# Performance work log

Hardware: AMD Instinct MI355X
Metric: run time of the kernel (lower is better)

Reference implementation:

```python
import jax, jax.numpy as jnp
import numpy as np

GRID_SIZE = 128
GAMMA = 200.0


def make_coordinate_grid(dim):
    # meshgrid over [-1, 1] x [-1, 1], shape [G, G, 2] with (x, y) ordering
    x = jnp.arange(dim, dtype=jnp.float32)
    y = jnp.arange(dim, dtype=jnp.float32)
    xx = jnp.broadcast_to(x[None, :], (dim, dim))
    yy = jnp.broadcast_to(y[:, None], (dim, dim))
    meshed = jnp.stack([xx, yy], axis=-1) / (dim - 1) * 2.0 - 1.0
    return meshed  # [G, G, 2]


def distance_transform(kps, mask, grid, gamma):
    # kps: [N, 2] points, mask: [N] bool (True -> segment dropped), grid: [G, G, 2]
    pi = kps[:-1]                      # [S, 2] segment start
    pj = kps[1:]                       # [S, 2] segment end
    v = pi - pj                        # [S, 2]
    u = grid[None, :, :, :] - pj[:, None, None, :]          # [S, G, G, 2]
    uv = jnp.einsum('sghd,sd->sgh', u, v)                   # [S, G, G]
    v_norm = jnp.sum(v * v, axis=-1)                        # [S]
    zero_seg = v_norm == 0.0
    v_safe = jnp.where(zero_seg, 1.0, v_norm)
    # clamp projection to [0,1]; degenerate segments (v_norm==0) fall back to uv
    # (which is exactly 0 there), matching torch's NaN masked_scatter fixup.
    rs = jnp.where(zero_seg[:, None, None], uv,
                   jnp.clip(uv / v_safe[:, None, None], 0.0, 1.0))  # [S, G, G]
    diff = u - rs[..., None] * v[:, None, None, :]          # [S, G, G, 2]
    betas = jnp.exp(-gamma * jnp.sum(diff * diff, axis=-1)) # [S, G, G]
    keep = (~mask[:-1]).astype(betas.dtype)                 # [S]
    betas = betas * keep[:, None, None]
    return jnp.max(betas, axis=0)                           # [G, G]


def setup_inputs() -> dict:
    key = jax.random.key(0)
    k1, k2, k3, k4 = jax.random.split(key, 4)
    N = 2048
    pred_xy = jax.random.uniform(k1, (N, 2), dtype=jnp.float32)
    pred_pen = (jax.random.uniform(k2, (N, 1)) < 0.1).astype(jnp.float32)
    gt_xy = jax.random.uniform(k3, (N, 2), dtype=jnp.float32)
    gt_pen = (jax.random.uniform(k4, (N, 1)) < 0.1).astype(jnp.float32)
    pred_coords = jnp.concatenate([pred_xy, pred_pen], axis=-1)  # [N, 3]
    gt_coords = jnp.concatenate([gt_xy, gt_pen], axis=-1)        # [N, 3]
    return {"pred_coords": pred_coords, "gt_coords": gt_coords}


def reference(pred_coords, gt_coords):
    grid = make_coordinate_grid(GRID_SIZE)
    mask_gt = gt_coords[:, -1] != 0.0
    gt_c = (gt_coords[:, :-1] - 0.5) * 2.0
    mask_pred = pred_coords[:, -1] > 0.5
    pred_c = (pred_coords[:, :-1] - 0.5) * 2.0
    gt_dist = distance_transform(gt_c, mask_gt, grid, GAMMA)
    pred_dist = distance_transform(pred_c, mask_pred, grid, GAMMA)
    dist_loss = jnp.mean((pred_dist - gt_dist) ** 2)
    return dist_loss
```

## Files before the change

kernel.cpp:

```cpp
#include <hip/hip_runtime.h>
#include <math.h>

#define GRID_DIM 128
#define NPIX 16384
#define NSEG 2047
#define NCHUNK 8
#define CHUNK 256
#define NTILE 64
#define GAMMA4 800.0f

typedef float v2f __attribute__((ext_vector_type(2)));


__global__ __launch_bounds__(256) void dist_min_kernel(
    const float* __restrict__ pred, const float* __restrict__ gt,
    unsigned int* __restrict__ ws_min)
{
    __shared__ float4 sA[2][CHUNK / 2];
    __shared__ float4 sB[2][CHUNK / 2];
    __shared__ float2 sC[2][CHUNK / 2];

    const int tid = threadIdx.x;
    const int bx = blockIdx.x;
    const int chunk = blockIdx.y;

    #pragma unroll
    for (int slot = tid; slot < 2 * CHUNK; slot += 256) {
        const int t = slot >> 8;
        const int sl = slot & (CHUNK - 1);
        const int s = chunk * CHUNK + sl;
        float pjx, pjy, vx, vy, inv;
        if (s < NSEG) {
            const float* src = t ? gt : pred;
            const float pix_ = src[3 * s + 0];
            const float piy_ = src[3 * s + 1];
            const float pen  = src[3 * s + 2];
            pjx = src[3 * s + 3];
            pjy = src[3 * s + 4];
            const bool masked = t ? (pen != 0.0f) : (pen > 0.5f);
            vx = pix_ - pjx;
            vy = piy_ - pjy;
            const float vn = vx * vx + vy * vy;
            inv = (vn == 0.0f) ? 0.0f : (1.0f / vn);
            if (masked) { pjx = 1e15f; pjy = 1e15f; vx = 0.0f; vy = 0.0f; inv = 0.0f; }
        } else {
            pjx = 1e15f; pjy = 1e15f; vx = 0.0f; vy = 0.0f; inv = 0.0f;
        }
        float* a = (float*)&sA[t][sl >> 1];
        float* b = (float*)&sB[t][sl >> 1];
        float* c = (float*)&sC[t][sl >> 1];
        const int k = sl & 1;
        a[k] = pjx; a[2 + k] = pjy;
        b[k] = vx;  b[2 + k] = vy;
        c[k] = inv;
    }
    __syncthreads();

    const int p = bx * 256 + tid;
    const float gx = (float)(p & (GRID_DIM - 1)) * (1.0f / 127.0f);
    const float gy = (float)(p >> 7) * (1.0f / 127.0f);
    const v2f gx2 = {gx, gx}, gy2 = {gy, gy};

    #pragma unroll
    for (int t = 0; t < 2; ++t) {
        float m = 3.0e38f;
        #pragma unroll 8
        for (int i = 0; i < CHUNK / 2; ++i) {
            const float4 A = sA[t][i];
            const float4 B = sB[t][i];
            const float2 C = sC[t][i];
            const v2f bx2 = {B.x, B.y}, by2 = {B.z, B.w};
            v2f ux = gx2 - (v2f){A.x, A.y};
            v2f uy = gy2 - (v2f){A.z, A.w};
            v2f uv = ux * bx2 + uy * by2;
            v2f rs = uv * (v2f){C.x, C.y};
            rs.x = fminf(fmaxf(rs.x, 0.0f), 1.0f);
            rs.y = fminf(fmaxf(rs.y, 0.0f), 1.0f);
            v2f dx = ux - rs * bx2;
            v2f dy = uy - rs * by2;
            v2f d2 = dx * dx + dy * dy;
            m = fminf(m, fminf(d2.x, d2.y));
        }
        atomicMin(&ws_min[t * NPIX + p], __float_as_uint(m));
    }
}

__global__ __launch_bounds__(1024) void dist_reduce_kernel(
    const float* __restrict__ ws_min, float* __restrict__ out)
{
    __shared__ float s_part[16];
    const int tid = threadIdx.x;
    float acc = 0.0f;
    #pragma unroll
    for (int i = 0; i < NPIX / 1024; ++i) {
        const int p = i * 1024 + tid;
        const float mp = ws_min[p];
        const float mg = ws_min[NPIX + p];
        const float d = __expf(-GAMMA4 * mp) - __expf(-GAMMA4 * mg);
        acc = fmaf(d, d, acc);
    }
    #pragma unroll
    for (int off = 32; off > 0; off >>= 1)
        acc += __shfl_down(acc, off, 64);
    if ((tid & 63) == 0) s_part[tid >> 6] = acc;
    __syncthreads();
    if (tid == 0) {
        float total = 0.0f;
        #pragma unroll
        for (int i = 0; i < 16; ++i) total += s_part[i];
        out[0] = total * (1.0f / (float)NPIX);
    }
}

extern "C" void kernel_launch(void* const* d_in, const int* in_sizes, int n_in,
                              void* d_out, int out_size, void* d_ws, size_t ws_size,
                              hipStream_t stream)
{
    const float* pred = (const float*)d_in[0];
    const float* gt   = (const float*)d_in[1];

    dim3 grid(NTILE, NCHUNK);
    dist_min_kernel<<<grid, 256, 0, stream>>>(pred, gt, (unsigned int*)d_ws);

    dist_reduce_kernel<<<1, 1024, 0, stream>>>((const float*)d_ws, (float*)d_out);
}
```

Measured before the change: 74.14 us.

## Split segments into more chunks and parallelize final reduction across blocks

The segment dimension is split into 32 chunks of 64 instead of 8 chunks of 256, giving four times as many blocks for better CU coverage, and the inner loop is fully unrolled. The final reduction now runs on 16 blocks with vectorized uint4 loads and combines block partials through atomicAdd, instead of a single 1024-thread block. The trade-off is four times more atomicMin traffic to the workspace. The reduction also now depends on the output being zeroed before launch.

```diff
diff --git a/kernel.cpp b/kernel.cpp
--- a/kernel.cpp
+++ b/kernel.cpp
@@ -4,8 +4,8 @@
 #define GRID_DIM 128
 #define NPIX 16384
 #define NSEG 2047
-#define NCHUNK 8
-#define CHUNK 256
+#define NCHUNK 32
+#define CHUNK 64
 #define NTILE 64
 #define GAMMA4 800.0f
 
@@ -24,10 +24,9 @@
     const int bx = blockIdx.x;
     const int chunk = blockIdx.y;
 
-    #pragma unroll
-    for (int slot = tid; slot < 2 * CHUNK; slot += 256) {
-        const int t = slot >> 8;
-        const int sl = slot & (CHUNK - 1);
+    if (tid < 2 * CHUNK) {
+        const int t = tid >> 6;
+        const int sl = tid & (CHUNK - 1);
         const int s = chunk * CHUNK + sl;
         float pjx, pjy, vx, vy, inv;
         if (s < NSEG) {
@@ -64,7 +63,7 @@
     #pragma unroll
     for (int t = 0; t < 2; ++t) {
         float m = 3.0e38f;
-        #pragma unroll 8
+        #pragma unroll
         for (int i = 0; i < CHUNK / 2; ++i) {
             const float4 A = sA[t][i];
             const float4 B = sB[t][i];
@@ -85,19 +84,25 @@
     }
 }
 
-__global__ __launch_bounds__(1024) void dist_reduce_kernel(
-    const float* __restrict__ ws_min, float* __restrict__ out)
+__global__ __launch_bounds__(256) void dist_reduce_kernel(
+    const uint4* __restrict__ ws_min, float* __restrict__ out)
 {
-    __shared__ float s_part[16];
+    __shared__ float s_part[4];
     const int tid = threadIdx.x;
-    float acc = 0.0f;
-    #pragma unroll
-    for (int i = 0; i < NPIX / 1024; ++i) {
-        const int p = i * 1024 + tid;
-        const float mp = ws_min[p];
-        const float mg = ws_min[NPIX + p];
-        const float d = __expf(-GAMMA4 * mp) - __expf(-GAMMA4 * mg);
-        acc = fmaf(d, d, acc);
+    const int q = blockIdx.x * 256 + tid;
+    const uint4 bp = ws_min[q];
+    const uint4 bg = ws_min[(NPIX / 4) + q];
+    float acc;
+    {
+        const float d0 = __expf(-GAMMA4 * __uint_as_float(bp.x))
+                       - __expf(-GAMMA4 * __uint_as_float(bg.x));
+        const float d1 = __expf(-GAMMA4 * __uint_as_float(bp.y))
+                       - __expf(-GAMMA4 * __uint_as_float(bg.y));
+        const float d2 = __expf(-GAMMA4 * __uint_as_float(bp.z))
+                       - __expf(-GAMMA4 * __uint_as_float(bg.z));
+        const float d3 = __expf(-GAMMA4 * __uint_as_float(bp.w))
+                       - __expf(-GAMMA4 * __uint_as_float(bg.w));
+        acc = d0 * d0 + d1 * d1 + d2 * d2 + d3 * d3;
     }
     #pragma unroll
     for (int off = 32; off > 0; off >>= 1)
@@ -105,10 +110,9 @@
     if ((tid & 63) == 0) s_part[tid >> 6] = acc;
     __syncthreads();
     if (tid == 0) {
-        float total = 0.0f;
-        #pragma unroll
-        for (int i = 0; i < 16; ++i) total += s_part[i];
-        out[0] = total * (1.0f / (float)NPIX);
+        const float blk = (s_part[0] + s_part[1] + s_part[2] + s_part[3])
+                          * (1.0f / (float)NPIX);
+        atomicAdd(out, blk);
     }
 }
 
@@ -122,5 +126,6 @@
     dim3 grid(NTILE, NCHUNK);
     dist_min_kernel<<<grid, 256, 0, stream>>>(pred, gt, (unsigned int*)d_ws);
 
-    dist_reduce_kernel<<<1, 1024, 0, stream>>>((const float*)d_ws, (float*)d_out);
+    dist_reduce_kernel<<<NPIX / 4 / 256, 256, 0, stream>>>(
+        (const uint4*)d_ws, (float*)d_out);
 }
```

After: 70.45 us. 1.05x faster.
